# Optimization experiments

Hardware: AMD Instinct MI355X
Metric: run time of the kernel (lower is better)

The kernel has to match this reference:

```python
import jax, jax.numpy as jnp
import numpy as np

N_NODES = 50000
N_EDGES = 600000
HID = 128
N_CONVS = 3
N_GRAPHS = 64


def setup_inputs() -> dict:
    key = jax.random.key(0)
    ks = jax.random.split(key, 8)
    scale = 1.0 / np.sqrt(HID)  # ~xavier
    node_attr = jax.random.normal(ks[0], (N_NODES, HID), dtype=jnp.float32)
    edge_attr = jax.random.normal(ks[1], (N_EDGES, HID), dtype=jnp.float32)
    edge_index = jax.random.randint(ks[2], (2, N_EDGES), 0, N_NODES, dtype=jnp.int32)
    batch = jnp.sort(jax.random.randint(ks[3], (N_NODES,), 0, N_GRAPHS, dtype=jnp.int32))
    W1 = jax.random.normal(ks[4], (N_CONVS, HID, HID), dtype=jnp.float32) * scale
    B1 = jnp.zeros((N_CONVS, HID), dtype=jnp.float32)
    W2 = jax.random.normal(ks[5], (N_CONVS, HID, HID), dtype=jnp.float32) * scale
    B2 = jnp.zeros((N_CONVS, HID), dtype=jnp.float32)
    return {"node_attr": node_attr, "edge_attr": edge_attr, "edge_index": edge_index,
            "batch": batch, "W1": W1, "B1": B1, "W2": W2, "B2": B2,
            "num_graphs": N_GRAPHS}


def _gine_conv(x, edge_index, edge_attr, w1, b1, w2, b2, eps=0.0):
    src, dst = edge_index[0], edge_index[1]
    # message: softplus(x_j + edge_attr), gathered from source nodes
    msg = jax.nn.softplus(x[src] + edge_attr)          # [E, H]
    agg = jax.ops.segment_sum(msg, dst, num_segments=x.shape[0])  # [N, H]
    out = agg + (1.0 + eps) * x
    # MLP: Linear -> softplus -> Linear (torch Linear: y = x @ W.T + b)
    h = jax.nn.softplus(out @ w1.T + b1)
    return h @ w2.T + b2


def reference(node_attr, edge_attr, edge_index, batch, W1, B1, W2, B2, num_graphs):
    x = node_attr
    for i in range(N_CONVS):
        h = _gine_conv(x, edge_index, edge_attr, W1[i], B1[i], W2[i], B2[i])
        if i < N_CONVS - 1:
            h = jax.nn.softplus(h)  # inter-layer activation
        x = h
    node_feature = x
    graph_feature = jax.ops.segment_sum(node_feature, batch, num_segments=num_graphs)
    return graph_feature, node_feature
```

## Files before the change

kernel.cpp:

```cpp
#include <hip/hip_runtime.h>
#include <math.h>

#define N_NODES 50000
#define N_EDGES 600000
#define HID 128
#define N_GRAPHS 64
#define BCAP 32
#define OVF_CAP 4096
#define PCHUNK 8
#define LDSP 136

typedef __attribute__((ext_vector_type(8))) short short8;
typedef __attribute__((ext_vector_type(4))) float floatx4;

__device__ __forceinline__ float softplus_f(float v) {
    return fmaxf(v, 0.0f) + __logf(1.0f + __expf(-fabsf(v)));
}
__device__ __forceinline__ unsigned short f2bf(float f) {
    unsigned u = __float_as_uint(f);
    u = (u + 0x7FFFu + ((u >> 16) & 1u)) >> 16;
    return (unsigned short)u;
}
__device__ __forceinline__ float bflo(unsigned u) { return __uint_as_float(u << 16); }
__device__ __forceinline__ float bfhi(unsigned u) { return __uint_as_float(u & 0xFFFF0000u); }

__global__ void pack_x(const float* __restrict__ xf, unsigned short* __restrict__ xb, int nelem4) {
    int t = blockIdx.x * 256 + threadIdx.x;
    if (t >= nelem4) return;
    float4 v = *(const float4*)(xf + (size_t)t * 4);
    unsigned o0 = (unsigned)f2bf(v.x) | ((unsigned)f2bf(v.y) << 16);
    unsigned o1 = (unsigned)f2bf(v.z) | ((unsigned)f2bf(v.w) << 16);
    *(uint2*)(xb + (size_t)t * 4) = make_uint2(o0, o1);
}

__global__ void build_buckets(const int* __restrict__ ei, int* __restrict__ cnt,
                              int2* __restrict__ bkt, int4* __restrict__ ovf) {
    int e = blockIdx.x * 256 + threadIdx.x;
    if (e >= N_EDGES) return;
    int src = ei[e];
    int dst = ei[N_EDGES + e];
    int slot = atomicAdd(&cnt[dst], 1);
    if (slot < BCAP) {
        bkt[(size_t)dst * BCAP + slot] = make_int2(e, src);
    } else {
        int k = atomicAdd(&cnt[N_NODES], 1);
        if (k < OVF_CAP) ovf[k] = make_int4(e, src, dst, 0);
    }
}

__global__ void __launch_bounds__(256) agg_kernel(const unsigned short* __restrict__ xb,
        const float* __restrict__ edge_attr, const int* __restrict__ cnt,
        const int2* __restrict__ bkt, const int4* __restrict__ ovf,
        unsigned short* __restrict__ outb) {
    int wave = blockIdx.x * 4 + (threadIdx.x >> 6);
    int lane = threadIdx.x & 63;
    int n = __builtin_amdgcn_readfirstlane(wave);
    if (n >= N_NODES) return;
    int h = lane >> 5;
    int l = lane & 31;
    int ctot = cnt[n];
    int c = ctot < BCAP ? ctot : BCAP;
    const int2* bk = bkt + (size_t)n * BCAP;
    float4 acc = make_float4(0.f, 0.f, 0.f, 0.f);
    int s = 0;
    for (; s + 4 <= c; s += 4) {
        int2 pA = bk[s + h];
        int2 pB = bk[s + 2 + h];
        float4 eA = *(const float4*)(edge_attr + (size_t)pA.x * HID + l * 4);
        uint2  xA = *(const uint2*)(xb + (size_t)pA.y * HID + l * 4);
        float4 eB = *(const float4*)(edge_attr + (size_t)pB.x * HID + l * 4);
        uint2  xB = *(const uint2*)(xb + (size_t)pB.y * HID + l * 4);
        acc.x += softplus_f(eA.x + bflo(xA.x)) + softplus_f(eB.x + bflo(xB.x));
        acc.y += softplus_f(eA.y + bfhi(xA.x)) + softplus_f(eB.y + bfhi(xB.x));
        acc.z += softplus_f(eA.z + bflo(xA.y)) + softplus_f(eB.z + bflo(xB.y));
        acc.w += softplus_f(eA.w + bfhi(xA.y)) + softplus_f(eB.w + bfhi(xB.y));
    }
    if (s + 2 <= c) {
        int2 p = bk[s + h];
        float4 ev = *(const float4*)(edge_attr + (size_t)p.x * HID + l * 4);
        uint2  xv = *(const uint2*)(xb + (size_t)p.y * HID + l * 4);
        acc.x += softplus_f(ev.x + bflo(xv.x));
        acc.y += softplus_f(ev.y + bfhi(xv.x));
        acc.z += softplus_f(ev.z + bflo(xv.y));
        acc.w += softplus_f(ev.w + bfhi(xv.y));
        s += 2;
    }
    if (s < c && h == 0) {
        int2 p = bk[s];
        float4 ev = *(const float4*)(edge_attr + (size_t)p.x * HID + l * 4);
        uint2  xv = *(const uint2*)(xb + (size_t)p.y * HID + l * 4);
        acc.x += softplus_f(ev.x + bflo(xv.x));
        acc.y += softplus_f(ev.y + bfhi(xv.x));
        acc.z += softplus_f(ev.z + bflo(xv.y));
        acc.w += softplus_f(ev.w + bfhi(xv.y));
    }
    if (ctot > BCAP) {
        int k = cnt[N_NODES]; if (k > OVF_CAP) k = OVF_CAP;
        for (int i = 0; i < k; i++) {
            int4 t = ovf[i];
            if (t.z == n && h == 0) {
                float4 ev = *(const float4*)(edge_attr + (size_t)t.x * HID + l * 4);
                uint2  xv = *(const uint2*)(xb + (size_t)t.y * HID + l * 4);
                acc.x += softplus_f(ev.x + bflo(xv.x));
                acc.y += softplus_f(ev.y + bfhi(xv.x));
                acc.z += softplus_f(ev.z + bflo(xv.y));
                acc.w += softplus_f(ev.w + bfhi(xv.y));
            }
        }
    }
    acc.x += __shfl(acc.x, l + 32);
    acc.y += __shfl(acc.y, l + 32);
    acc.z += __shfl(acc.z, l + 32);
    acc.w += __shfl(acc.w, l + 32);
    if (h == 0) {
        uint2 xn = *(const uint2*)(xb + (size_t)n * HID + l * 4);
        acc.x += bflo(xn.x); acc.y += bfhi(xn.x);
        acc.z += bflo(xn.y); acc.w += bfhi(xn.y);
        unsigned o0 = (unsigned)f2bf(acc.x) | ((unsigned)f2bf(acc.y) << 16);
        unsigned o1 = (unsigned)f2bf(acc.z) | ((unsigned)f2bf(acc.w) << 16);
        *(uint2*)(outb + (size_t)n * HID + l * 4) = make_uint2(o0, o1);
    }
}

__global__ void pack_w(const float* __restrict__ W1, const float* __restrict__ W2,
                       unsigned short* __restrict__ pw) {
    int t = blockIdx.x * 256 + threadIdx.x;
    if (t >= 6 * 32 * 64) return;
    int lane = t & 63;
    int tile = (t >> 6) & 31;
    int mat = t >> 11;
    int kt = tile >> 3, nt = tile & 7;
    const float* W = (mat & 1) ? W2 : W1;
    W += (size_t)(mat >> 1) * HID * HID;
    int n = nt * 16 + (lane & 15);
    int kbase = kt * 32 + (lane >> 4) * 8;
    short8 v;
    #pragma unroll
    for (int j = 0; j < 8; j++) v[j] = (short)f2bf(W[(size_t)n * HID + kbase + j]);
    *((short8*)(pw + (size_t)t * 8)) = v;
}

__global__ void __launch_bounds__(256) mlp_fused(const unsigned short* __restrict__ A,
        const unsigned short* __restrict__ pw1, const unsigned short* __restrict__ pw2,
        const float* __restrict__ b1, const float* __restrict__ b2,
        void* __restrict__ outp, int final_layer) {
    __shared__ __align__(16) unsigned short hl[2][16][LDSP];
    int wave = threadIdx.x >> 6, lane = threadIdx.x & 63;
    int rt = wave >> 1, ch = wave & 1;
    int m = lane & 15, q = lane >> 4;
    int r0 = blockIdx.x * 32 + rt * 16;
    int row = r0 + m;
    bool rv = row < N_NODES;
    short8 zf = {0, 0, 0, 0, 0, 0, 0, 0};
    floatx4 zero = {0.f, 0.f, 0.f, 0.f};
    floatx4 acc[4];
    #pragma unroll
    for (int t = 0; t < 4; t++) acc[t] = zero;
    const short8* ar = (const short8*)(A + (size_t)row * HID + q * 8);
    const short8* w1 = (const short8*)pw1;
    #pragma unroll
    for (int kt = 0; kt < 4; kt++) {
        short8 af = rv ? ar[kt * 4] : zf;
        const short8* wp = w1 + (size_t)(kt * 8 + ch * 4) * 64 + lane;
        #pragma unroll
        for (int t = 0; t < 4; t++)
            acc[t] = __builtin_amdgcn_mfma_f32_16x16x32_bf16(af, wp[t * 64], acc[t], 0, 0, 0);
    }
    #pragma unroll
    for (int t = 0; t < 4; t++) {
        int col = ch * 64 + t * 16 + m;
        float bb = b1[col];
        #pragma unroll
        for (int i = 0; i < 4; i++)
            hl[rt][q * 4 + i][col] = f2bf(softplus_f(acc[t][i] + bb));
    }
    __syncthreads();
    #pragma unroll
    for (int t = 0; t < 4; t++) acc[t] = zero;
    const short8* w2 = (const short8*)pw2;
    #pragma unroll
    for (int kt = 0; kt < 4; kt++) {
        short8 af = *(const short8*)&hl[rt][m][kt * 32 + q * 8];
        const short8* wp = w2 + (size_t)(kt * 8 + ch * 4) * 64 + lane;
        #pragma unroll
        for (int t = 0; t < 4; t++)
            acc[t] = __builtin_amdgcn_mfma_f32_16x16x32_bf16(af, wp[t * 64], acc[t], 0, 0, 0);
    }
    if (final_layer) {
        float* out = (float*)outp;
        #pragma unroll
        for (int t = 0; t < 4; t++) {
            int col = ch * 64 + t * 16 + m;
            float bb = b2[col];
            #pragma unroll
            for (int i = 0; i < 4; i++) {
                int r = r0 + q * 4 + i;
                if (r < N_NODES) out[(size_t)r * HID + col] = acc[t][i] + bb;
            }
        }
    } else {
        __syncthreads();
        #pragma unroll
        for (int t = 0; t < 4; t++) {
            int col = ch * 64 + t * 16 + m;
            float bb = b2[col];
            #pragma unroll
            for (int i = 0; i < 4; i++)
                hl[rt][q * 4 + i][col] = f2bf(softplus_f(acc[t][i] + bb));
        }
        __syncthreads();
        unsigned short* outb = (unsigned short*)outp;
        int tid = threadIdx.x;
        int orow = tid >> 3, cseg = (tid & 7) * 16;
        int gr = blockIdx.x * 32 + orow;
        if (gr < N_NODES) {
            uint4 v0 = *(const uint4*)&hl[orow >> 4][orow & 15][cseg];
            uint4 v1 = *(const uint4*)&hl[orow >> 4][orow & 15][cseg + 8];
            *(uint4*)(outb + (size_t)gr * HID + cseg) = v0;
            *(uint4*)(outb + (size_t)gr * HID + cseg + 8) = v1;
        }
    }
}

__global__ void find_bounds(const int* __restrict__ batch, int* __restrict__ start) {
    int n = blockIdx.x * 256 + threadIdx.x;
    if (n >= N_NODES) return;
    int bn = batch[n];
    int bp = (n == 0) ? -1 : batch[n - 1];
    for (int g = bp + 1; g <= bn; g++) start[g] = n;
    if (n == N_NODES - 1)
        for (int g = bn + 1; g <= N_GRAPHS; g++) start[g] = N_NODES;
}

__global__ void pool_partial(const float* __restrict__ nf, const int* __restrict__ start,
                             float* __restrict__ part) {
    int g = blockIdx.x >> 3, c = blockIdx.x & (PCHUNK - 1);
    int j = threadIdx.x;
    int s = start[g], e = start[g + 1];
    int len = e - s;
    int b0 = s + (len * c) / PCHUNK;
    int b1 = s + (len * (c + 1)) / PCHUNK;
    float acc = 0.f;
    for (int n = b0; n < b1; n++) acc += nf[(size_t)n * HID + j];
    part[(size_t)blockIdx.x * HID + j] = acc;
}

__global__ void pool_final(const float* __restrict__ part, float* __restrict__ gout) {
    int g = blockIdx.x, j = threadIdx.x;
    float acc = 0.f;
    #pragma unroll
    for (int c = 0; c < PCHUNK; c++) acc += part[(size_t)(g * PCHUNK + c) * HID + j];
    gout[(size_t)g * HID + j] = acc;
}

extern "C" void kernel_launch(void* const* d_in, const int* in_sizes, int n_in,
                              void* d_out, int out_size, void* d_ws, size_t ws_size,
                              hipStream_t stream) {
    const float* node_attr = (const float*)d_in[0];
    const float* edge_attr = (const float*)d_in[1];
    const int*   ei        = (const int*)d_in[2];
    const int*   batch     = (const int*)d_in[3];
    const float* W1        = (const float*)d_in[4];
    const float* B1        = (const float*)d_in[5];
    const float* W2        = (const float*)d_in[6];
    const float* B2        = (const float*)d_in[7];

    float* gout    = (float*)d_out;
    float* nodeout = (float*)d_out + N_GRAPHS * HID;

    const size_t NH = (size_t)N_NODES * HID;
    unsigned short* nab  = (unsigned short*)d_ws;
    unsigned short* bufA = nab + NH;
    unsigned short* bufB = bufA + NH;
    int*   cnt = (int*)(bufB + NH);
    int4*  ovf = (int4*)(cnt + 50004);
    int2*  bkt = (int2*)(ovf + OVF_CAP);
    unsigned short* pw = (unsigned short*)(bkt + (size_t)N_NODES * BCAP);
    int*   startb = (int*)(pw + 6 * 16384);
    float* part = (float*)(startb + 68);

    hipMemsetAsync(cnt, 0, (size_t)50001 * sizeof(int), stream);
    build_buckets<<<(N_EDGES + 255) / 256, 256, 0, stream>>>(ei, cnt, bkt, ovf);
    pack_w<<<(6 * 32 * 64 + 255) / 256, 256, 0, stream>>>(W1, W2, pw);
    pack_x<<<((int)(NH / 4) + 255) / 256, 256, 0, stream>>>(node_attr, nab, (int)(NH / 4));
    find_bounds<<<(N_NODES + 255) / 256, 256, 0, stream>>>(batch, startb);

    const int agg_blocks = (N_NODES + 3) / 4;
    const int mlp_blocks = (N_NODES + 31) / 32;

    const unsigned short* xcur = nab;
    for (int i = 0; i < 3; i++) {
        agg_kernel<<<agg_blocks, 256, 0, stream>>>(xcur, edge_attr, cnt, bkt, ovf, bufA);
        void* outp = (i == 2) ? (void*)nodeout : (void*)bufB;
        mlp_fused<<<mlp_blocks, 256, 0, stream>>>(bufA,
                pw + (size_t)(i * 2) * 16384, pw + (size_t)(i * 2 + 1) * 16384,
                B1 + (size_t)i * HID, B2 + (size_t)i * HID, outp, (i == 2) ? 1 : 0);
        xcur = bufB;
    }
    pool_partial<<<N_GRAPHS * PCHUNK, HID, 0, stream>>>(nodeout, startb, part);
    pool_final<<<N_GRAPHS, HID, 0, stream>>>(part, gout);
}
```

Baseline: 746.5 us.

## Pre-sort edge features by destination into bf16 CSR layout for aggregation

Builds a CSR-style ordering of edges by destination node with a single-block prefix scan over the bucket counts. A new pass then permutes edge_attr into that order and packs it to bf16, along with a sorted source-index array. The three aggregation passes then read edge features contiguously at half the bytes, instead of gathering fp32 rows by edge id. In exchange it adds setup kernels (a serial-ish 1024-thread scan and a 600k-row permute), a large workspace buffer, and extra bf16 rounding of edge_attr.

```diff
diff --git a/kernel.cpp b/kernel.cpp
--- a/kernel.cpp
+++ b/kernel.cpp
@@ -23,6 +23,12 @@
 }
 __device__ __forceinline__ float bflo(unsigned u) { return __uint_as_float(u << 16); }
 __device__ __forceinline__ float bfhi(unsigned u) { return __uint_as_float(u & 0xFFFF0000u); }
+__device__ __forceinline__ uint2 bfpack4(float4 v) {
+    uint2 o;
+    o.x = (unsigned)f2bf(v.x) | ((unsigned)f2bf(v.y) << 16);
+    o.y = (unsigned)f2bf(v.z) | ((unsigned)f2bf(v.w) << 16);
+    return o;
+}
 
 __global__ void pack_x(const float* __restrict__ xf, unsigned short* __restrict__ xb, int nelem4) {
     int t = blockIdx.x * 256 + threadIdx.x;
@@ -33,25 +39,72 @@
     *(uint2*)(xb + (size_t)t * 4) = make_uint2(o0, o1);
 }
 
-__global__ void build_buckets(const int* __restrict__ ei, int* __restrict__ cnt,
-                              int2* __restrict__ bkt, int4* __restrict__ ovf) {
+__global__ void build_buckets2(const int* __restrict__ ei, int* __restrict__ cnt,
+                               int2* __restrict__ sed, int4* __restrict__ ovf) {
     int e = blockIdx.x * 256 + threadIdx.x;
     if (e >= N_EDGES) return;
     int src = ei[e];
     int dst = ei[N_EDGES + e];
     int slot = atomicAdd(&cnt[dst], 1);
     if (slot < BCAP) {
-        bkt[(size_t)dst * BCAP + slot] = make_int2(e, src);
+        sed[e] = make_int2(dst, slot);
     } else {
+        sed[e] = make_int2(-1, 0);
         int k = atomicAdd(&cnt[N_NODES], 1);
         if (k < OVF_CAP) ovf[k] = make_int4(e, src, dst, 0);
     }
 }
 
-__global__ void __launch_bounds__(256) agg_kernel(const unsigned short* __restrict__ xb,
+__global__ void __launch_bounds__(1024) scan_off(const int* __restrict__ cnt,
+                                                 int* __restrict__ off) {
+    __shared__ int ls[1024];
+    int t = threadIdx.x;
+    const int PER = (N_NODES + 1023) / 1024;
+    int base = t * PER;
+    int sum = 0;
+    for (int i = 0; i < PER; i++) {
+        int n = base + i;
+        if (n < N_NODES) { int c = cnt[n]; if (c > BCAP) c = BCAP; sum += c; }
+    }
+    ls[t] = sum;
+    __syncthreads();
+    for (int d = 1; d < 1024; d <<= 1) {
+        int v = (t >= d) ? ls[t - d] : 0;
+        __syncthreads();
+        ls[t] += v;
+        __syncthreads();
+    }
+    int run = (t > 0) ? ls[t - 1] : 0;
+    for (int i = 0; i < PER; i++) {
+        int n = base + i;
+        if (n < N_NODES) {
+            off[n] = run;
+            int c = cnt[n]; if (c > BCAP) c = BCAP;
+            run += c;
+        }
+    }
+}
+
+__global__ void __launch_bounds__(256) permute_e(const float* __restrict__ ef,
+        const int2* __restrict__ sed, const int* __restrict__ ei,
+        const int* __restrict__ off, unsigned short* __restrict__ ebs,
+        int* __restrict__ srcs) {
+    int e = blockIdx.x * 8 + (threadIdx.x >> 5);
+    if (e >= N_EDGES) return;
+    int l = threadIdx.x & 31;
+    int2 ds = sed[e];
+    if (ds.x < 0) return;
+    int pos = off[ds.x] + ds.y;
+    if (l == 0) srcs[pos] = ei[e];
+    float4 v = *(const float4*)(ef + (size_t)e * HID + l * 4);
+    *(uint2*)(ebs + (size_t)pos * HID + l * 4) = bfpack4(v);
+}
+
+__global__ void __launch_bounds__(256) agg_seq(const unsigned short* __restrict__ xb,
         const float* __restrict__ edge_attr, const int* __restrict__ cnt,
-        const int2* __restrict__ bkt, const int4* __restrict__ ovf,
-        unsigned short* __restrict__ outb) {
+        const int* __restrict__ srcs, const int4* __restrict__ ovf,
+        unsigned short* __restrict__ outb,
+        const unsigned short* __restrict__ ebs, const int* __restrict__ off) {
     int wave = blockIdx.x * 4 + (threadIdx.x >> 6);
     int lane = threadIdx.x & 63;
     int n = __builtin_amdgcn_readfirstlane(wave);
@@ -60,39 +113,41 @@
     int l = lane & 31;
     int ctot = cnt[n];
     int c = ctot < BCAP ? ctot : BCAP;
-    const int2* bk = bkt + (size_t)n * BCAP;
+    int p0 = (c > 0) ? off[n] : 0;
+    const int* sr = srcs + p0;
+    const unsigned short* er = ebs + (size_t)p0 * HID;
     float4 acc = make_float4(0.f, 0.f, 0.f, 0.f);
     int s = 0;
     for (; s + 4 <= c; s += 4) {
-        int2 pA = bk[s + h];
-        int2 pB = bk[s + 2 + h];
-        float4 eA = *(const float4*)(edge_attr + (size_t)pA.x * HID + l * 4);
-        uint2  xA = *(const uint2*)(xb + (size_t)pA.y * HID + l * 4);
-        float4 eB = *(const float4*)(edge_attr + (size_t)pB.x * HID + l * 4);
-        uint2  xB = *(const uint2*)(xb + (size_t)pB.y * HID + l * 4);
-        acc.x += softplus_f(eA.x + bflo(xA.x)) + softplus_f(eB.x + bflo(xB.x));
-        acc.y += softplus_f(eA.y + bfhi(xA.x)) + softplus_f(eB.y + bfhi(xB.x));
-        acc.z += softplus_f(eA.z + bflo(xA.y)) + softplus_f(eB.z + bflo(xB.y));
-        acc.w += softplus_f(eA.w + bfhi(xA.y)) + softplus_f(eB.w + bfhi(xB.y));
+        int srcA = sr[s + h];
+        int srcB = sr[s + 2 + h];
+        uint2 eA = *(const uint2*)(er + (size_t)(s + h) * HID + l * 4);
+        uint2 xA = *(const uint2*)(xb + (size_t)srcA * HID + l * 4);
+        uint2 eB = *(const uint2*)(er + (size_t)(s + 2 + h) * HID + l * 4);
+        uint2 xB = *(const uint2*)(xb + (size_t)srcB * HID + l * 4);
+        acc.x += softplus_f(bflo(eA.x) + bflo(xA.x)) + softplus_f(bflo(eB.x) + bflo(xB.x));
+        acc.y += softplus_f(bfhi(eA.x) + bfhi(xA.x)) + softplus_f(bfhi(eB.x) + bfhi(xB.x));
+        acc.z += softplus_f(bflo(eA.y) + bflo(xA.y)) + softplus_f(bflo(eB.y) + bflo(xB.y));
+        acc.w += softplus_f(bfhi(eA.y) + bfhi(xA.y)) + softplus_f(bfhi(eB.y) + bfhi(xB.y));
     }
     if (s + 2 <= c) {
-        int2 p = bk[s + h];
-        float4 ev = *(const float4*)(edge_attr + (size_t)p.x * HID + l * 4);
-        uint2  xv = *(const uint2*)(xb + (size_t)p.y * HID + l * 4);
-        acc.x += softplus_f(ev.x + bflo(xv.x));
-        acc.y += softplus_f(ev.y + bfhi(xv.x));
-        acc.z += softplus_f(ev.z + bflo(xv.y));
-        acc.w += softplus_f(ev.w + bfhi(xv.y));
+        int sc = sr[s + h];
+        uint2 ev = *(const uint2*)(er + (size_t)(s + h) * HID + l * 4);
+        uint2 xv = *(const uint2*)(xb + (size_t)sc * HID + l * 4);
+        acc.x += softplus_f(bflo(ev.x) + bflo(xv.x));
+        acc.y += softplus_f(bfhi(ev.x) + bfhi(xv.x));
+        acc.z += softplus_f(bflo(ev.y) + bflo(xv.y));
+        acc.w += softplus_f(bfhi(ev.y) + bfhi(xv.y));
         s += 2;
     }
     if (s < c && h == 0) {
-        int2 p = bk[s];
-        float4 ev = *(const float4*)(edge_attr + (size_t)p.x * HID + l * 4);
-        uint2  xv = *(const uint2*)(xb + (size_t)p.y * HID + l * 4);
-        acc.x += softplus_f(ev.x + bflo(xv.x));
-        acc.y += softplus_f(ev.y + bfhi(xv.x));
-        acc.z += softplus_f(ev.z + bflo(xv.y));
-        acc.w += softplus_f(ev.w + bfhi(xv.y));
+        int sc = sr[s];
+        uint2 ev = *(const uint2*)(er + (size_t)s * HID + l * 4);
+        uint2 xv = *(const uint2*)(xb + (size_t)sc * HID + l * 4);
+        acc.x += softplus_f(bflo(ev.x) + bflo(xv.x));
+        acc.y += softplus_f(bfhi(ev.x) + bfhi(xv.x));
+        acc.z += softplus_f(bflo(ev.y) + bflo(xv.y));
+        acc.w += softplus_f(bfhi(ev.y) + bfhi(xv.y));
     }
     if (ctot > BCAP) {
         int k = cnt[N_NODES]; if (k > OVF_CAP) k = OVF_CAP;
@@ -272,15 +327,20 @@
     unsigned short* nab  = (unsigned short*)d_ws;
     unsigned short* bufA = nab + NH;
     unsigned short* bufB = bufA + NH;
-    int*   cnt = (int*)(bufB + NH);
+    unsigned short* ebs  = bufB + NH;
+    int*   cnt = (int*)(ebs + (size_t)N_EDGES * HID);
     int4*  ovf = (int4*)(cnt + 50004);
-    int2*  bkt = (int2*)(ovf + OVF_CAP);
-    unsigned short* pw = (unsigned short*)(bkt + (size_t)N_NODES * BCAP);
+    int2*  sed = (int2*)(ovf + OVF_CAP);
+    int*   srcs = (int*)(sed + N_EDGES);
+    int*   off = srcs + N_EDGES;
+    unsigned short* pw = (unsigned short*)(off + 50000);
     int*   startb = (int*)(pw + 6 * 16384);
     float* part = (float*)(startb + 68);
 
     hipMemsetAsync(cnt, 0, (size_t)50001 * sizeof(int), stream);
-    build_buckets<<<(N_EDGES + 255) / 256, 256, 0, stream>>>(ei, cnt, bkt, ovf);
+    build_buckets2<<<(N_EDGES + 255) / 256, 256, 0, stream>>>(ei, cnt, sed, ovf);
+    scan_off<<<1, 1024, 0, stream>>>(cnt, off);
+    permute_e<<<(N_EDGES + 7) / 8, 256, 0, stream>>>(edge_attr, sed, ei, off, ebs, srcs);
     pack_w<<<(6 * 32 * 64 + 255) / 256, 256, 0, stream>>>(W1, W2, pw);
     pack_x<<<((int)(NH / 4) + 255) / 256, 256, 0, stream>>>(node_attr, nab, (int)(NH / 4));
     find_bounds<<<(N_NODES + 255) / 256, 256, 0, stream>>>(batch, startb);
@@ -290,7 +350,8 @@
 
     const unsigned short* xcur = nab;
     for (int i = 0; i < 3; i++) {
-        agg_kernel<<<agg_blocks, 256, 0, stream>>>(xcur, edge_attr, cnt, bkt, ovf, bufA);
+        agg_seq<<<agg_blocks, 256, 0, stream>>>(xcur, edge_attr, cnt, srcs, ovf,
+                bufA, ebs, off);
         void* outp = (i == 2) ? (void*)nodeout : (void*)bufB;
         mlp_fused<<<mlp_blocks, 256, 0, stream>>>(bufA,
                 pw + (size_t)(i * 2) * 16384, pw + (size_t)(i * 2 + 1) * 16384,
```

Result: slower. 866.5 us (+16.1%).

## Fuse all stages into one persistent cooperative kernel with grid syncs

Applied to the files above, without the earlier changes.

Replaces the memset and the roughly twelve separate kernel launches (bucket build, packing, three agg/MLP layer pairs, pooling) with a single cooperative persistent kernel. Stages are separated by grid.sync() and run as grid-stride loops over a grid sized from occupancy. This removes per-launch gaps and the memset call. In exchange it adds grid-barrier cost, and the persistent grid (capped at 1536 blocks under launch bounds of 256 threads, 6 blocks) may cut occupancy and load balance in the memory-bound aggregation.

```diff
diff --git a/kernel.cpp b/kernel.cpp
--- a/kernel.cpp
+++ b/kernel.cpp
@@ -1,5 +1,8 @@
 #include <hip/hip_runtime.h>
+#include <hip/hip_cooperative_groups.h>
 #include <math.h>
+
+namespace cg = cooperative_groups;
 
 #define N_NODES 50000
 #define N_EDGES 600000
@@ -9,6 +12,7 @@
 #define OVF_CAP 4096
 #define PCHUNK 8
 #define LDSP 136
+#define MLPB ((N_NODES + 31) / 32)
 
 typedef __attribute__((ext_vector_type(8))) short short8;
 typedef __attribute__((ext_vector_type(4))) float floatx4;
@@ -23,39 +27,33 @@
 }
 __device__ __forceinline__ float bflo(unsigned u) { return __uint_as_float(u << 16); }
 __device__ __forceinline__ float bfhi(unsigned u) { return __uint_as_float(u & 0xFFFF0000u); }
-
-__global__ void pack_x(const float* __restrict__ xf, unsigned short* __restrict__ xb, int nelem4) {
-    int t = blockIdx.x * 256 + threadIdx.x;
-    if (t >= nelem4) return;
-    float4 v = *(const float4*)(xf + (size_t)t * 4);
-    unsigned o0 = (unsigned)f2bf(v.x) | ((unsigned)f2bf(v.y) << 16);
-    unsigned o1 = (unsigned)f2bf(v.z) | ((unsigned)f2bf(v.w) << 16);
-    *(uint2*)(xb + (size_t)t * 4) = make_uint2(o0, o1);
-}
-
-__global__ void build_buckets(const int* __restrict__ ei, int* __restrict__ cnt,
-                              int2* __restrict__ bkt, int4* __restrict__ ovf) {
-    int e = blockIdx.x * 256 + threadIdx.x;
-    if (e >= N_EDGES) return;
-    int src = ei[e];
-    int dst = ei[N_EDGES + e];
-    int slot = atomicAdd(&cnt[dst], 1);
-    if (slot < BCAP) {
-        bkt[(size_t)dst * BCAP + slot] = make_int2(e, src);
-    } else {
-        int k = atomicAdd(&cnt[N_NODES], 1);
-        if (k < OVF_CAP) ovf[k] = make_int4(e, src, dst, 0);
-    }
-}
-
-__global__ void __launch_bounds__(256) agg_kernel(const unsigned short* __restrict__ xb,
-        const float* __restrict__ edge_attr, const int* __restrict__ cnt,
-        const int2* __restrict__ bkt, const int4* __restrict__ ovf,
-        unsigned short* __restrict__ outb) {
-    int wave = blockIdx.x * 4 + (threadIdx.x >> 6);
-    int lane = threadIdx.x & 63;
-    int n = __builtin_amdgcn_readfirstlane(wave);
+__device__ __forceinline__ uint2 bfpack4(float4 v) {
+    uint2 o;
+    o.x = (unsigned)f2bf(v.x) | ((unsigned)f2bf(v.y) << 16);
+    o.y = (unsigned)f2bf(v.z) | ((unsigned)f2bf(v.w) << 16);
+    return o;
+}
+
+struct Params {
+    const float* node_attr;
+    const float* edge_attr;
+    const int*   ei;
+    const int*   batch;
+    const float* W1; const float* B1;
+    const float* W2; const float* B2;
+    float* gout; float* nodeout;
+    unsigned short* nab; unsigned short* bufA; unsigned short* bufB;
+    int* cnt; int4* ovf; int2* bkt;
+    unsigned short* pw;
+    int* startb; float* part;
+};
+
+__device__ __forceinline__ void agg_node(int n, int lane,
+        const unsigned short* __restrict__ xb, const float* __restrict__ edge_attr,
+        const int* __restrict__ cnt, const int2* __restrict__ bkt,
+        const int4* __restrict__ ovf, unsigned short* __restrict__ outb) {
     if (n >= N_NODES) return;
+    n = __builtin_amdgcn_readfirstlane(n);
     int h = lane >> 5;
     int l = lane & 31;
     int ctot = cnt[n];
@@ -122,33 +120,16 @@
     }
 }
 
-__global__ void pack_w(const float* __restrict__ W1, const float* __restrict__ W2,
-                       unsigned short* __restrict__ pw) {
-    int t = blockIdx.x * 256 + threadIdx.x;
-    if (t >= 6 * 32 * 64) return;
-    int lane = t & 63;
-    int tile = (t >> 6) & 31;
-    int mat = t >> 11;
-    int kt = tile >> 3, nt = tile & 7;
-    const float* W = (mat & 1) ? W2 : W1;
-    W += (size_t)(mat >> 1) * HID * HID;
-    int n = nt * 16 + (lane & 15);
-    int kbase = kt * 32 + (lane >> 4) * 8;
-    short8 v;
-    #pragma unroll
-    for (int j = 0; j < 8; j++) v[j] = (short)f2bf(W[(size_t)n * HID + kbase + j]);
-    *((short8*)(pw + (size_t)t * 8)) = v;
-}
-
-__global__ void __launch_bounds__(256) mlp_fused(const unsigned short* __restrict__ A,
+__device__ __forceinline__ void mlp_tile(int bx, int tid,
+        unsigned short (&hl)[2][16][LDSP],
+        const unsigned short* __restrict__ A,
         const unsigned short* __restrict__ pw1, const unsigned short* __restrict__ pw2,
         const float* __restrict__ b1, const float* __restrict__ b2,
         void* __restrict__ outp, int final_layer) {
-    __shared__ __align__(16) unsigned short hl[2][16][LDSP];
-    int wave = threadIdx.x >> 6, lane = threadIdx.x & 63;
+    int wave = tid >> 6, lane = tid & 63;
     int rt = wave >> 1, ch = wave & 1;
     int m = lane & 15, q = lane >> 4;
-    int r0 = blockIdx.x * 32 + rt * 16;
+    int r0 = bx * 32 + rt * 16;
     int row = r0 + m;
     bool rv = row < N_NODES;
     short8 zf = {0, 0, 0, 0, 0, 0, 0, 0};
@@ -210,9 +191,8 @@
         }
         __syncthreads();
         unsigned short* outb = (unsigned short*)outp;
-        int tid = threadIdx.x;
         int orow = tid >> 3, cseg = (tid & 7) * 16;
-        int gr = blockIdx.x * 32 + orow;
+        int gr = bx * 32 + orow;
         if (gr < N_NODES) {
             uint4 v0 = *(const uint4*)&hl[orow >> 4][orow & 15][cseg];
             uint4 v1 = *(const uint4*)&hl[orow >> 4][orow & 15][cseg + 8];
@@ -222,81 +202,141 @@
     }
 }
 
-__global__ void find_bounds(const int* __restrict__ batch, int* __restrict__ start) {
-    int n = blockIdx.x * 256 + threadIdx.x;
-    if (n >= N_NODES) return;
-    int bn = batch[n];
-    int bp = (n == 0) ? -1 : batch[n - 1];
-    for (int g = bp + 1; g <= bn; g++) start[g] = n;
-    if (n == N_NODES - 1)
-        for (int g = bn + 1; g <= N_GRAPHS; g++) start[g] = N_NODES;
-}
-
-__global__ void pool_partial(const float* __restrict__ nf, const int* __restrict__ start,
-                             float* __restrict__ part) {
-    int g = blockIdx.x >> 3, c = blockIdx.x & (PCHUNK - 1);
-    int j = threadIdx.x;
-    int s = start[g], e = start[g + 1];
-    int len = e - s;
-    int b0 = s + (len * c) / PCHUNK;
-    int b1 = s + (len * (c + 1)) / PCHUNK;
-    float acc = 0.f;
-    for (int n = b0; n < b1; n++) acc += nf[(size_t)n * HID + j];
-    part[(size_t)blockIdx.x * HID + j] = acc;
-}
-
-__global__ void pool_final(const float* __restrict__ part, float* __restrict__ gout) {
-    int g = blockIdx.x, j = threadIdx.x;
-    float acc = 0.f;
-    #pragma unroll
-    for (int c = 0; c < PCHUNK; c++) acc += part[(size_t)(g * PCHUNK + c) * HID + j];
-    gout[(size_t)g * HID + j] = acc;
+__global__ void __launch_bounds__(256, 6) gin_all(Params p) {
+    cg::grid_group grid = cg::this_grid();
+    __shared__ __align__(16) unsigned short hl[2][16][LDSP];
+    const int tid  = threadIdx.x;
+    const int G    = gridDim.x;
+    const int gtid = blockIdx.x * 256 + tid;
+    const int NT   = G * 256;
+
+    for (int i = gtid; i < N_NODES + 1; i += NT) p.cnt[i] = 0;
+    grid.sync();
+
+    for (int e = gtid; e < N_EDGES; e += NT) {
+        int src = p.ei[e];
+        int dst = p.ei[N_EDGES + e];
+        int slot = atomicAdd(&p.cnt[dst], 1);
+        if (slot < BCAP) {
+            p.bkt[(size_t)dst * BCAP + slot] = make_int2(e, src);
+        } else {
+            int k = atomicAdd(&p.cnt[N_NODES], 1);
+            if (k < OVF_CAP) p.ovf[k] = make_int4(e, src, dst, 0);
+        }
+    }
+    for (int t = gtid; t < (int)((size_t)N_NODES * HID / 4); t += NT) {
+        float4 v = *(const float4*)(p.node_attr + (size_t)t * 4);
+        *(uint2*)(p.nab + (size_t)t * 4) = bfpack4(v);
+    }
+    for (int t = gtid; t < 6 * 32 * 64; t += NT) {
+        int lane = t & 63;
+        int tile = (t >> 6) & 31;
+        int mat = t >> 11;
+        int kt = tile >> 3, nt = tile & 7;
+        const float* W = (mat & 1) ? p.W2 : p.W1;
+        W += (size_t)(mat >> 1) * HID * HID;
+        int n = nt * 16 + (lane & 15);
+        int kbase = kt * 32 + (lane >> 4) * 8;
+        short8 v;
+        #pragma unroll
+        for (int j = 0; j < 8; j++) v[j] = (short)f2bf(W[(size_t)n * HID + kbase + j]);
+        *((short8*)(p.pw + (size_t)t * 8)) = v;
+    }
+    for (int n = gtid; n < N_NODES; n += NT) {
+        int bn = p.batch[n];
+        int bp = (n == 0) ? -1 : p.batch[n - 1];
+        for (int g = bp + 1; g <= bn; g++) p.startb[g] = n;
+        if (n == N_NODES - 1)
+            for (int g = bn + 1; g <= N_GRAPHS; g++) p.startb[g] = N_NODES;
+    }
+    grid.sync();
+
+    const unsigned short* xcur = p.nab;
+    const int wv0 = blockIdx.x * 4 + (tid >> 6);
+    const int lane = tid & 63;
+    for (int layer = 0; layer < 3; layer++) {
+        for (int n = wv0; n < N_NODES; n += G * 4)
+            agg_node(n, lane, xcur, p.edge_attr, p.cnt, p.bkt, p.ovf, p.bufA);
+        grid.sync();
+
+        const unsigned short* pw1 = p.pw + (size_t)(layer * 2) * 16384;
+        const unsigned short* pw2 = p.pw + (size_t)(layer * 2 + 1) * 16384;
+        const float* b1 = p.B1 + (size_t)layer * HID;
+        const float* b2 = p.B2 + (size_t)layer * HID;
+        int fin = (layer == 2);
+        void* outp = fin ? (void*)p.nodeout : (void*)p.bufB;
+        for (int vb = blockIdx.x; vb < MLPB; vb += G) {
+            __syncthreads();
+            mlp_tile(vb, tid, hl, p.bufA, pw1, pw2, b1, b2, outp, fin);
+        }
+        grid.sync();
+        xcur = p.bufB;
+    }
+
+    {
+        int sub = tid >> 7, j = tid & 127;
+        for (int vb = blockIdx.x * 2 + sub; vb < N_GRAPHS * PCHUNK; vb += G * 2) {
+            int g = vb >> 3, c = vb & (PCHUNK - 1);
+            int s = p.startb[g], e = p.startb[g + 1];
+            int len = e - s;
+            int b0 = s + (len * c) / PCHUNK;
+            int b1i = s + (len * (c + 1)) / PCHUNK;
+            float acc = 0.f;
+            for (int n = b0; n < b1i; n++) acc += p.nodeout[(size_t)n * HID + j];
+            p.part[(size_t)vb * HID + j] = acc;
+        }
+    }
+    grid.sync();
+
+    {
+        int sub = tid >> 7, j = tid & 127;
+        for (int g = blockIdx.x * 2 + sub; g < N_GRAPHS; g += G * 2) {
+            float acc = 0.f;
+            #pragma unroll
+            for (int c = 0; c < PCHUNK; c++)
+                acc += p.part[(size_t)(g * PCHUNK + c) * HID + j];
+            p.gout[(size_t)g * HID + j] = acc;
+        }
+    }
 }
 
 extern "C" void kernel_launch(void* const* d_in, const int* in_sizes, int n_in,
                               void* d_out, int out_size, void* d_ws, size_t ws_size,
                               hipStream_t stream) {
-    const float* node_attr = (const float*)d_in[0];
-    const float* edge_attr = (const float*)d_in[1];
-    const int*   ei        = (const int*)d_in[2];
-    const int*   batch     = (const int*)d_in[3];
-    const float* W1        = (const float*)d_in[4];
-    const float* B1        = (const float*)d_in[5];
-    const float* W2        = (const float*)d_in[6];
-    const float* B2        = (const float*)d_in[7];
-
-    float* gout    = (float*)d_out;
-    float* nodeout = (float*)d_out + N_GRAPHS * HID;
+    Params p;
+    p.node_attr = (const float*)d_in[0];
+    p.edge_attr = (const float*)d_in[1];
+    p.ei        = (const int*)d_in[2];
+    p.batch     = (const int*)d_in[3];
+    p.W1        = (const float*)d_in[4];
+    p.B1        = (const float*)d_in[5];
+    p.W2        = (const float*)d_in[6];
+    p.B2        = (const float*)d_in[7];
+
+    p.gout    = (float*)d_out;
+    p.nodeout = (float*)d_out + N_GRAPHS * HID;
 
     const size_t NH = (size_t)N_NODES * HID;
-    unsigned short* nab  = (unsigned short*)d_ws;
-    unsigned short* bufA = nab + NH;
-    unsigned short* bufB = bufA + NH;
-    int*   cnt = (int*)(bufB + NH);
-    int4*  ovf = (int4*)(cnt + 50004);
-    int2*  bkt = (int2*)(ovf + OVF_CAP);
-    unsigned short* pw = (unsigned short*)(bkt + (size_t)N_NODES * BCAP);
-    int*   startb = (int*)(pw + 6 * 16384);
-    float* part = (float*)(startb + 68);
-
-    hipMemsetAsync(cnt, 0, (size_t)50001 * sizeof(int), stream);
-    build_buckets<<<(N_EDGES + 255) / 256, 256, 0, stream>>>(ei, cnt, bkt, ovf);
-    pack_w<<<(6 * 32 * 64 + 255) / 256, 256, 0, stream>>>(W1, W2, pw);
-    pack_x<<<((int)(NH / 4) + 255) / 256, 256, 0, stream>>>(node_attr, nab, (int)(NH / 4));
-    find_bounds<<<(N_NODES + 255) / 256, 256, 0, stream>>>(batch, startb);
-
-    const int agg_blocks = (N_NODES + 3) / 4;
-    const int mlp_blocks = (N_NODES + 31) / 32;
-
-    const unsigned short* xcur = nab;
-    for (int i = 0; i < 3; i++) {
-        agg_kernel<<<agg_blocks, 256, 0, stream>>>(xcur, edge_attr, cnt, bkt, ovf, bufA);
-        void* outp = (i == 2) ? (void*)nodeout : (void*)bufB;
-        mlp_fused<<<mlp_blocks, 256, 0, stream>>>(bufA,
-                pw + (size_t)(i * 2) * 16384, pw + (size_t)(i * 2 + 1) * 16384,
-                B1 + (size_t)i * HID, B2 + (size_t)i * HID, outp, (i == 2) ? 1 : 0);
-        xcur = bufB;
-    }
-    pool_partial<<<N_GRAPHS * PCHUNK, HID, 0, stream>>>(nodeout, startb, part);
-    pool_final<<<N_GRAPHS, HID, 0, stream>>>(part, gout);
-}
+    p.nab  = (unsigned short*)d_ws;
+    p.bufA = p.nab + NH;
+    p.bufB = p.bufA + NH;
+    p.cnt  = (int*)(p.bufB + NH);
+    p.ovf  = (int4*)(p.cnt + 50004);
+    p.bkt  = (int2*)(p.ovf + OVF_CAP);
+    p.pw   = (unsigned short*)(p.bkt + (size_t)N_NODES * BCAP);
+    p.startb = (int*)(p.pw + 6 * 16384);
+    p.part = (float*)(p.startb + 68);
+
+    static int maxb = -1;
+    if (maxb < 0) {
+        int mb = 0;
+        hipError_t err = hipOccupancyMaxActiveBlocksPerMultiprocessor(
+                &mb, (const void*)gin_all, 256, 0);
+        maxb = (err == hipSuccess && mb > 0) ? mb : 4;
+    }
+    int G = maxb * 256;
+    if (G > 1536) G = 1536;
+
+    void* kp[1] = { (void*)&p };
+    hipLaunchCooperativeKernel((const void*)gin_all, dim3(G), dim3(256), kp, 0, stream);
+}
```

Result: slower. 1.746 ms (+133.9%).
